# Optimization experiments

Measured on AMD Instinct MI355X. Metric: run time of the kernel, lower is better.

## Reference

```python
import jax, jax.numpy as jnp
import numpy as np

MODES = 20
WIDTH = 64
EPS = 1e-5


def spectral_conv(x, w1, w2, m1, m2):
    # x: [B, C, H, W] real; w1, w2: [Ci, Co, m1, m2, 2] (real/imag)
    B, C, H, W = x.shape
    xf = jnp.fft.rfft2(x, norm='ortho')  # [B, C, H, W//2+1] complex
    w1c = w1[..., 0] + 1j * w1[..., 1]
    w2c = w2[..., 0] + 1j * w2[..., 1]
    m1 = min(m1, H)
    m2 = min(m2, W // 2 + 1)
    top = jnp.einsum('bixy,ioxy->boxy', xf[:, :, :m1, :m2], w1c[:, :, :m1, :m2])
    bot = jnp.einsum('bixy,ioxy->boxy', xf[:, :, -m1:, :m2], w2c[:, :, :m1, :m2])
    out = jnp.zeros((B, w1.shape[1], H, W // 2 + 1), dtype=xf.dtype)
    out = out.at[:, :, :m1, :m2].set(top)
    out = out.at[:, :, H - m1:, :m2].set(bot)
    return jnp.fft.irfft2(out, s=(H, W), norm='ortho')


def batchnorm2d(x, gamma, beta):
    # training-mode BN over (B, H, W) per channel; x: [B, C, H, W]
    mean = jnp.mean(x, axis=(0, 2, 3), keepdims=True)
    var = jnp.var(x, axis=(0, 2, 3), keepdims=True)
    xn = (x - mean) * jax.lax.rsqrt(var + EPS)
    return xn * gamma[None, :, None, None] + beta[None, :, None, None]


def setup_inputs() -> dict:
    key = jax.random.key(0)
    ks = jax.random.split(key, 12)
    B, H, W, Tin2 = 8, 256, 256, 12
    scale = 1.0 / (WIDTH * WIDTH)
    return {
        'x': jax.random.normal(ks[0], (B, H, W, Tin2), jnp.float32),
        'fc0_w': jax.random.normal(ks[1], (Tin2, WIDTH), jnp.float32) * 0.1,
        'fc0_b': jnp.zeros((WIDTH,), jnp.float32),
        'sw1': scale * jax.random.normal(ks[2], (4, WIDTH, WIDTH, MODES, MODES, 2), jnp.float32),
        'sw2': scale * jax.random.normal(ks[3], (4, WIDTH, WIDTH, MODES, MODES, 2), jnp.float32),
        'cw': jax.random.normal(ks[4], (4, WIDTH, WIDTH), jnp.float32) * 0.1,
        'cb': jnp.zeros((4, WIDTH), jnp.float32),
        'bng': jnp.ones((4, WIDTH), jnp.float32),
        'bnb': jnp.zeros((4, WIDTH), jnp.float32),
        'fc1_w': jax.random.normal(ks[5], (WIDTH, 128), jnp.float32) * 0.1,
        'fc1_b': jnp.zeros((128,), jnp.float32),
        'fc2_w': jax.random.normal(ks[6], (128, 1), jnp.float32) * 0.1,
        'fc2_b': jnp.zeros((1,), jnp.float32),
    }


def reference(x, fc0_w, fc0_b, sw1, sw2, cw, cb, bng, bnb, fc1_w, fc1_b, fc2_w, fc2_b):
    # lift: [B, H, W, Tin+2] -> [B, C, H, W]
    h = jnp.einsum('bhwt,tc->bhwc', x, fc0_w) + fc0_b
    h = jnp.transpose(h, (0, 3, 1, 2))
    for l in range(4):
        spec = spectral_conv(h, sw1[l], sw2[l], MODES, MODES)
        lin = jnp.einsum('bihw,oi->bohw', h, cw[l]) + cb[l][None, :, None, None]
        h = batchnorm2d(spec + lin, bng[l], bnb[l])
        if l < 3:
            h = jax.nn.relu(h)
    h = jnp.transpose(h, (0, 2, 3, 1))  # [B, H, W, C]
    h = jax.nn.relu(jnp.einsum('bhwc,cd->bhwd', h, fc1_w) + fc1_b)
    out = jnp.einsum('bhwd,de->bhwe', h, fc2_w) + fc2_b
    return out
```

## Files before the change

### kernel.cpp

```cpp
#include <hip/hip_runtime.h>
#include <hip/hip_bf16.h>


__device__ __forceinline__ void gll16(const float* gsrc, float* ldst) {
    __builtin_amdgcn_global_load_lds(
        (const __attribute__((address_space(1))) void*)gsrc,
        (__attribute__((address_space(3))) void*)ldst, 16, 0, 0);
}

__device__ __forceinline__ unsigned bfp(float x) {
    unsigned u = __float_as_uint(x);
    return (u + 0x7fffu + ((u >> 16) & 1u)) >> 16;
}

__global__ __launch_bounds__(256) void init_k(const float* __restrict__ cw,
                                              float* __restrict__ costab, float* __restrict__ sintab,
                                              float* __restrict__ EAt, float* __restrict__ Tw,
                                              float* __restrict__ cwT, float* __restrict__ stats) {
    int idx = blockIdx.x * 256 + threadIdx.x;
    const float PH = 6.28318530717958647692f / 256.f;
    if (idx < 256) {
        float s, c; sincosf(idx * PH, &s, &c);
        costab[idx] = c; sintab[idx] = s;
    } else if (idx < 256 + 10240) {
        int e = idx - 256;
        int n = e >> 8, w = e & 255, ky = n >> 1;
        int r = (ky * w) & 255;
        float s, c; sincosf(r * PH, &s, &c);
        EAt[e] = (n & 1) ? -s : c;
    } else if (idx < 256 + 20480) {
        int e = idx - 10496;
        int kp = e >> 8, w = e & 255;
        int ky = kp >> 1, p = kp & 1;
        int r = (ky * w) & 255;
        float s, c; sincosf(r * PH, &s, &c);
        float v;
        if (ky == 0) v = p ? 0.f : (1.f / 16.f);
        else         v = p ? (-2.f / 16.f) * s : (2.f / 16.f) * c;
        Tw[e] = v;
    } else if (idx < 256 + 20480 + 16384) {
        int e = idx - 20736;
        int l = e >> 12, r2 = e & 4095;
        int i = r2 >> 6, o = r2 & 63;
        cwT[e] = cw[(l << 12) + (o << 6) + i];
    } else if (idx < 256 + 20480 + 16384 + 2048) {
        stats[idx - 37120] = 0.f;
    }
}

__global__ __launch_bounds__(256) void wtrans_k(const float* __restrict__ sw1,
                                                const float* __restrict__ sw2,
                                                unsigned int* __restrict__ wt) {
    int gid = blockIdx.x * 4 + (threadIdx.x >> 6);
    int o = threadIdx.x & 63;
    int xyc = gid % 25;
    int i = (gid / 25) & 63;
    int t2 = gid / 1600;
    const float* src = ((t2 & 1) ? sw2 : sw1) + (t2 >> 1) * 3276800;
    const float* sp = src + ((i * 64 + o) * 400 + xyc * 16) * 2;
    unsigned int* dp = wt + (size_t)(t2 * 400 + xyc * 16) * 4096 + i * 64 + o;
#pragma unroll
    for (int j = 0; j < 16; ++j) {
        float re = sp[2 * j], im = sp[2 * j + 1];
        dp[(size_t)j * 4096] = bfp(re) | (bfp(im) << 16);
    }
}

__global__ __launch_bounds__(256) void fc0_k(const float* __restrict__ x,
                                             const float* __restrict__ w,
                                             const float* __restrict__ bias,
                                             float* __restrict__ outb) {
    __shared__ float ws[768];
    __shared__ float bs[64];
    int tid = threadIdx.x;
    for (int i = tid; i < 768; i += 256) ws[i] = w[i];
    if (tid < 64) bs[tid] = bias[tid];
    __syncthreads();
    int pix = blockIdx.x * 256 + tid;
    int b = pix >> 16, hw = pix & 65535;
    float xv[12];
#pragma unroll
    for (int t = 0; t < 12; ++t) xv[t] = x[pix * 12 + t];
    int base = (b << 22) + hw;
    for (int c = 0; c < 64; ++c) {
        float a = bs[c];
#pragma unroll
        for (int t = 0; t < 12; ++t) a += xv[t] * ws[t * 64 + c];
        outb[base + (c << 16)] = a;
    }
}

__global__ __launch_bounds__(128) void dftw_k(float* __restrict__ X,
                                              const float* __restrict__ EAt,
                                              float* __restrict__ T,
                                              const float* __restrict__ statsl,
                                              const float* __restrict__ g,
                                              const float* __restrict__ bt,
                                              int fuse) {
    __shared__ __align__(16) float Xs[32 * 68];
    __shared__ __align__(16) float Est[40 * 32];
    int tid = threadIdx.x;
    int tm = tid >> 3, tn = tid & 7;
    int row0 = blockIdx.x << 6;
    float sc = 1.f, sh = 0.f;
    if (fuse) {
        int c = (row0 >> 8) & 63;
        float ssum = statsl[c] + statsl[128 + c] + statsl[256 + c] + statsl[384 + c];
        float ssq  = statsl[64 + c] + statsl[192 + c] + statsl[320 + c] + statsl[448 + c];
        float mean = ssum * (1.f / 524288.f);
        float var = ssq * (1.f / 524288.f) - mean * mean;
        sc = g[c] * rsqrtf(var + 1e-5f);
        sh = bt[c] - mean * sc;
    }
    float acc[4][5];
#pragma unroll
    for (int i = 0; i < 4; ++i)
#pragma unroll
        for (int j = 0; j < 5; ++j) acc[i][j] = 0.f;

#pragma unroll 1
    for (int kc = 0; kc < 256; kc += 32) {
        __syncthreads();
#pragma unroll
        for (int r = 0; r < 4; ++r) {
            int m = tm + (r << 4);
            float4 v = *(const float4*)&X[(row0 + m) * 256 + kc + (tn << 2)];
            if (fuse) {
                v.x = fmaxf(fmaf(v.x, sc, sh), 0.f);
                v.y = fmaxf(fmaf(v.y, sc, sh), 0.f);
                v.z = fmaxf(fmaf(v.z, sc, sh), 0.f);
                v.w = fmaxf(fmaf(v.w, sc, sh), 0.f);
                *(float4*)&X[(row0 + m) * 256 + kc + (tn << 2)] = v;
            }
            int kb = tn << 2;
            Xs[(kb + 0) * 68 + m] = v.x;
            Xs[(kb + 1) * 68 + m] = v.y;
            Xs[(kb + 2) * 68 + m] = v.z;
            Xs[(kb + 3) * 68 + m] = v.w;
        }
        for (int i = tid; i < 1280; i += 128) Est[i] = EAt[((i >> 5) << 8) + kc + (i & 31)];
        __syncthreads();
#pragma unroll 1
        for (int k4 = 0; k4 < 8; ++k4) {
            float4 e0 = *(const float4*)&Est[(tn * 5 + 0) * 32 + (k4 << 2)];
            float4 e1 = *(const float4*)&Est[(tn * 5 + 1) * 32 + (k4 << 2)];
            float4 e2 = *(const float4*)&Est[(tn * 5 + 2) * 32 + (k4 << 2)];
            float4 e3 = *(const float4*)&Est[(tn * 5 + 3) * 32 + (k4 << 2)];
            float4 e4 = *(const float4*)&Est[(tn * 5 + 4) * 32 + (k4 << 2)];
#pragma unroll
            for (int c2 = 0; c2 < 4; ++c2) {
                float4 a = *(const float4*)&Xs[((k4 << 2) + c2) * 68 + (tm << 2)];
                float ev0 = ((const float*)&e0)[c2];
                float ev1 = ((const float*)&e1)[c2];
                float ev2 = ((const float*)&e2)[c2];
                float ev3 = ((const float*)&e3)[c2];
                float ev4 = ((const float*)&e4)[c2];
                acc[0][0] += a.x * ev0; acc[1][0] += a.y * ev0; acc[2][0] += a.z * ev0; acc[3][0] += a.w * ev0;
                acc[0][1] += a.x * ev1; acc[1][1] += a.y * ev1; acc[2][1] += a.z * ev1; acc[3][1] += a.w * ev1;
                acc[0][2] += a.x * ev2; acc[1][2] += a.y * ev2; acc[2][2] += a.z * ev2; acc[3][2] += a.w * ev2;
                acc[0][3] += a.x * ev3; acc[1][3] += a.y * ev3; acc[2][3] += a.z * ev3; acc[3][3] += a.w * ev3;
                acc[0][4] += a.x * ev4; acc[1][4] += a.y * ev4; acc[2][4] += a.z * ev4; acc[3][4] += a.w * ev4;
            }
        }
    }
#pragma unroll
    for (int i = 0; i < 4; ++i) {
        int row = row0 + (tm << 2) + i;
#pragma unroll
        for (int j = 0; j < 5; ++j) T[row * 40 + tn * 5 + j] = acc[i][j];
    }
}

__global__ __launch_bounds__(1024) void dfth_k(const float* __restrict__ T,
                                               const float* __restrict__ ct, const float* __restrict__ st,
                                               float* __restrict__ XF) {
    __shared__ __align__(16) float Ts[10240];
    __shared__ float cts[256], sts[256];
    __shared__ float part[3][1600];
    int tid = threadIdx.x;
    int bc = blockIdx.x;
    for (int i = tid; i < 10240; i += 1024) Ts[i] = T[bc * 10240 + i];
    if (tid < 256) { cts[tid] = ct[tid]; sts[tid] = st[tid]; }
    __syncthreads();
    int gq = tid >> 8, t2 = tid & 255;
    float ar0 = 0, ai0 = 0, ar1 = 0, ai1 = 0, ar2 = 0, ai2 = 0, ar3 = 0, ai3 = 0;
    int kxi = t2 / 5, kyg = t2 % 5;
    if (t2 < 200) {
        int kxa = kxi < 20 ? kxi : kxi + 216;
        int h0 = gq << 6;
        int r = (kxa * h0) & 255;
#pragma unroll 1
        for (int hh = 0; hh < 64; ++hh) {
            int h = h0 + hh;
            float cc = cts[r], sv = sts[r];
            r = (r + kxa) & 255;
            float4 v0 = *(const float4*)&Ts[h * 40 + (kyg << 3)];
            float4 v1 = *(const float4*)&Ts[h * 40 + (kyg << 3) + 4];
            ar0 += v0.x * cc + v0.y * sv;  ai0 += v0.y * cc - v0.x * sv;
            ar1 += v0.z * cc + v0.w * sv;  ai1 += v0.w * cc - v0.z * sv;
            ar2 += v1.x * cc + v1.y * sv;  ai2 += v1.y * cc - v1.x * sv;
            ar3 += v1.z * cc + v1.w * sv;  ai3 += v1.w * cc - v1.z * sv;
        }
        if (gq) {
            float* p = &part[gq - 1][t2 * 8];
            p[0] = ar0; p[1] = ai0; p[2] = ar1; p[3] = ai1;
            p[4] = ar2; p[5] = ai2; p[6] = ar3; p[7] = ai3;
        }
    }
    __syncthreads();
    if (gq == 0 && t2 < 200) {
#pragma unroll
        for (int j = 0; j < 3; ++j) {
            const float* p = &part[j][t2 * 8];
            ar0 += p[0]; ai0 += p[1]; ar1 += p[2]; ai1 += p[3];
            ar2 += p[4]; ai2 += p[5]; ar3 += p[6]; ai3 += p[7];
        }
        int b = bc >> 6, c = bc & 63;
        const float s = 1.f / 256.f;
        int A = (b * 40 + kxi) * 20 + (kyg << 2);
        float2* O = (float2*)XF;
        O[(A + 0) * 64 + c] = make_float2(ar0 * s, ai0 * s);
        O[(A + 1) * 64 + c] = make_float2(ar1 * s, ai1 * s);
        O[(A + 2) * 64 + c] = make_float2(ar2 * s, ai2 * s);
        O[(A + 3) * 64 + c] = make_float2(ar3 * s, ai3 * s);
    }
}

__global__ __launch_bounds__(512) void eins_t_k(const float* __restrict__ XF,
                                                const unsigned int* __restrict__ wtl,
                                                float* __restrict__ YF) {
    __shared__ float xfs[1024];
    int tid = threadIdx.x;
    int x = blockIdx.x / 20, y = blockIdx.x % 20;
    for (int i = tid; i < 1024; i += 512) {
        int b = i >> 7, rr = i & 127;
        xfs[i] = XF[(b * 40 + x) * 2560 + y * 128 + rr];
    }
    __syncthreads();
    int b = tid >> 6, o = tid & 63;
    const unsigned int* wp = wtl + (size_t)(((x < 20 ? 0 : 400) + (x % 20) * 20 + y)) * 4096 + o;
    float ar = 0.f, ai = 0.f;
#pragma unroll 8
    for (int i = 0; i < 64; ++i) {
        unsigned int wv = wp[i << 6];
        float wr = __uint_as_float(wv << 16);
        float wi = __uint_as_float(wv & 0xffff0000u);
        float xr = xfs[(b << 7) + (i << 1)];
        float xi = xfs[(b << 7) + (i << 1) + 1];
        ar += xr * wr - xi * wi;
        ai += xr * wi + xi * wr;
    }
    ((float2*)YF)[((b * 40 + x) * 20 + y) * 64 + o] = make_float2(ar, ai);
}

__global__ __launch_bounds__(512) void eins_k(const float* __restrict__ XF,
                                              const float* __restrict__ w1, const float* __restrict__ w2,
                                              float* __restrict__ YF) {
    __shared__ float xfs[1024];
    int tid = threadIdx.x;
    int x = blockIdx.x / 20, y = blockIdx.x % 20;
    for (int i = tid; i < 1024; i += 512) {
        int b = i >> 7, rr = i & 127;
        xfs[i] = XF[(b * 40 + x) * 2560 + y * 128 + rr];
    }
    __syncthreads();
    int b = tid >> 6, o = tid & 63;
    const float* wp = (x < 20) ? (w1 + (x * 20 + y) * 2) : (w2 + ((x - 20) * 20 + y) * 2);
    float ar = 0.f, ai = 0.f;
#pragma unroll 8
    for (int i = 0; i < 64; ++i) {
        float2 wv = *(const float2*)&wp[(i * 64 + o) * 800];
        float xr = xfs[(b << 7) + (i << 1)];
        float xi = xfs[(b << 7) + (i << 1) + 1];
        ar += xr * wv.x - xi * wv.y;
        ai += xr * wv.y + xi * wv.x;
    }
    ((float2*)YF)[((b * 40 + x) * 20 + y) * 64 + o] = make_float2(ar, ai);
}

__global__ __launch_bounds__(256) void idfth_k(const float* __restrict__ YF,
                                               const float* __restrict__ ct, const float* __restrict__ st,
                                               float* __restrict__ Z) {
    __shared__ __align__(16) float yfs[1600];
    __shared__ float cts[256], sts[256];
    int tid = threadIdx.x;
    int bc = blockIdx.x;
    int b = bc >> 6, co = bc & 63;
    for (int i = tid; i < 800; i += 256) {
        int kx = i / 20, ky = i % 20;
        float2 v = ((const float2*)YF)[((b * 40 + kx) * 20 + ky) * 64 + co];
        yfs[kx * 40 + 2 * ky] = v.x;
        yfs[kx * 40 + 2 * ky + 1] = v.y;
    }
    cts[tid] = ct[tid]; sts[tid] = st[tid];
    __syncthreads();
    int h = tid;
    float accr[20], acci[20];
#pragma unroll
    for (int q = 0; q < 20; ++q) { accr[q] = 0.f; acci[q] = 0.f; }
#pragma unroll 1
    for (int kxi = 0; kxi < 40; ++kxi) {
        int kxa = kxi < 20 ? kxi : kxi + 216;
        int r = (kxa * h) & 255;
        float cc = cts[r], sv = sts[r];
#pragma unroll
        for (int q = 0; q < 10; ++q) {
            float4 v = *(const float4*)&yfs[kxi * 40 + (q << 2)];
            accr[2 * q]     += v.x * cc - v.y * sv;  acci[2 * q]     += v.x * sv + v.y * cc;
            accr[2 * q + 1] += v.z * cc - v.w * sv;  acci[2 * q + 1] += v.z * sv + v.w * cc;
        }
    }
    const float s = 1.f / 16.f;
    int base = (bc * 256 + h) * 40;
#pragma unroll
    for (int q = 0; q < 10; ++q) {
        float4 o4;
        o4.x = accr[2 * q] * s;     o4.y = acci[2 * q] * s;
        o4.z = accr[2 * q + 1] * s; o4.w = acci[2 * q + 1] * s;
        *(float4*)&Z[base + (q << 2)] = o4;
    }
}

#define FMA2(I, AV, J, B4) \
    acc[I][J].x += (AV) * B4.x; acc[I][J].y += (AV) * B4.y; \
    acc[I][J].z += (AV) * B4.z; acc[I][J].w += (AV) * B4.w;

#define FMA_COL(J, B4) \
    FMA2(0, a0.x, J, B4) FMA2(1, a0.y, J, B4) FMA2(2, a0.z, J, B4) FMA2(3, a0.w, J, B4) \
    FMA2(4, a1.x, J, B4) FMA2(5, a1.y, J, B4) FMA2(6, a1.z, J, B4) FMA2(7, a1.w, J, B4)

#define FMA_COLU(J, B4) \
    FMA2(0, au0.x, J, B4) FMA2(1, au0.y, J, B4) FMA2(2, au0.z, J, B4) FMA2(3, au0.w, J, B4) \
    FMA2(4, au1.x, J, B4) FMA2(5, au1.y, J, B4) FMA2(6, au1.z, J, B4) FMA2(7, au1.w, J, B4)

#define FMA_COLD(J, B4) \
    FMA2(0, ad0.x, J, B4) FMA2(1, ad0.y, J, B4) FMA2(2, ad0.z, J, B4) FMA2(3, ad0.w, J, B4) \
    FMA2(4, ad1.x, J, B4) FMA2(5, ad1.y, J, B4) FMA2(6, ad1.z, J, B4) FMA2(7, ad1.w, J, B4)

__global__ __launch_bounds__(256) void speclin_k(const float* __restrict__ hin,
                                                 const float* __restrict__ Z,
                                                 const float* __restrict__ cwTl,
                                                 const float* __restrict__ Tw,
                                                 const float* __restrict__ cbl,
                                                 float* __restrict__ pre,
                                                 float* __restrict__ statsl) {
    __shared__ __align__(16) float As[64 * 68];
    __shared__ __align__(16) float Zs[80 * 64];
    __shared__ __align__(16) float Bs[2][4096];
    int tid = threadIdx.x;
    int bid = blockIdx.x;
    int b = bid >> 7, hp = bid & 127;
    int h0 = hp << 1;
    int to = tid >> 5, tw = tid & 31;
    int o0 = to << 3;

#pragma unroll
    for (int t = 0; t < 4; ++t) {
        int i4 = tid + (t << 8);
        float4 v = *(const float4*)&cwTl[i4 << 2];
        float* d = &As[(i4 >> 4) * 68 + ((i4 & 15) << 2)];
        d[0] = v.x; d[1] = v.y; d[2] = v.z; d[3] = v.w;
    }
#pragma unroll
    for (int t = 0; t < 5; ++t) {
        int i4 = tid + (t << 8);
        int q = i4 % 10;
        int u = i4 / 10;
        int o = u & 63, r = u >> 6;
        float4 v = *(const float4*)&Z[(((b << 6) + o) * 256 + h0 + r) * 40 + (q << 2)];
        int base = ((r * 40 + (q << 2)) << 6) + o;
        Zs[base]       = v.x;
        Zs[base + 64]  = v.y;
        Zs[base + 128] = v.z;
        Zs[base + 192] = v.w;
    }
    const float* hrow = hin + (size_t)((((b << 6) << 8) + h0) << 8);
#pragma unroll
    for (int t = 0; t < 4; ++t) {
        int i4 = tid + (t << 8);
        int k = i4 >> 7, n4 = i4 & 127, r = n4 >> 6, w4 = n4 & 63;
        gll16(&hrow[(k << 16) + (r << 8) + (w4 << 2)], &Bs[0][i4 << 2]);
    }
    __syncthreads();

    float4 acc[8][4];
#pragma unroll
    for (int i = 0; i < 8; ++i)
#pragma unroll
        for (int j = 0; j < 4; ++j) acc[i][j] = make_float4(0.f, 0.f, 0.f, 0.f);

    int cur = 0;
#pragma unroll 1
    for (int ch = 0; ch < 8; ++ch) {
        if (ch < 7) {
#pragma unroll
            for (int t = 0; t < 4; ++t) {
                int i4 = tid + (t << 8);
                int k = i4 >> 7, n4 = i4 & 127, r = n4 >> 6, w4 = n4 & 63;
                gll16(&hrow[((((ch + 1) << 3) + k) << 16) + (r << 8) + (w4 << 2)],
                      &Bs[cur ^ 1][i4 << 2]);
            }
        } else {
#pragma unroll
            for (int t = 0; t < 2; ++t) {
                int i4 = tid + (t << 8);
                gll16(&Tw[i4 << 2], &Bs[cur ^ 1][i4 << 2]);
            }
        }
        const float* Bc = Bs[cur];
        const float* Ac = &As[(ch << 3) * 68 + o0];
#pragma unroll 1
        for (int kk = 0; kk < 8; ++kk) {
            float4 a0 = *(const float4*)&Ac[kk * 68];
            float4 a1 = *(const float4*)&Ac[kk * 68 + 4];
            float4 b0 = *(const float4*)&Bc[(kk << 9) + (tw << 2)];
            float4 b1 = *(const float4*)&Bc[(kk << 9) + 128 + (tw << 2)];
            FMA_COL(0, b0)
            FMA_COL(1, b1)
            float4 b2 = *(const float4*)&Bc[(kk << 9) + 256 + (tw << 2)];
            float4 b3 = *(const float4*)&Bc[(kk << 9) + 384 + (tw << 2)];
            FMA_COL(2, b2)
            FMA_COL(3, b3)
        }
        __syncthreads();
        cur ^= 1;
    }

#pragma unroll 1
    for (int ch = 0; ch < 5; ++ch) {
        if (ch < 4) {
#pragma unroll
            for (int t = 0; t < 2; ++t) {
                int i4 = tid + (t << 8);
                gll16(&Tw[(((ch + 1) << 3) << 8) + (i4 << 2)], &Bs[cur ^ 1][i4 << 2]);
            }
        }
        const float* Bc = Bs[cur];
#pragma unroll 1
        for (int kk = 0; kk < 8; ++kk) {
            int kp = (ch << 3) + kk;
            float4 b0 = *(const float4*)&Bc[(kk << 8) + (tw << 2)];
            float4 b1 = *(const float4*)&Bc[(kk << 8) + 128 + (tw << 2)];
            float4 au0 = *(const float4*)&Zs[(kp << 6) + o0];
            float4 au1 = *(const float4*)&Zs[(kp << 6) + o0 + 4];
            FMA_COLU(0, b0)
            FMA_COLU(1, b1)
            float4 ad0 = *(const float4*)&Zs[((40 + kp) << 6) + o0];
            float4 ad1 = *(const float4*)&Zs[((40 + kp) << 6) + o0 + 4];
            FMA_COLD(2, b0)
            FMA_COLD(3, b1)
        }
        __syncthreads();
        cur ^= 1;
    }

    float* srep = statsl + ((bid & 3) << 7);
#pragma unroll
    for (int i = 0; i < 8; ++i) {
        float cbv = cbl[o0 + i];
        float sum = 0.f, sq = 0.f;
#pragma unroll
        for (int j = 0; j < 4; ++j) {
            float4 v = acc[i][j];
            v.x += cbv; v.y += cbv; v.z += cbv; v.w += cbv;
            int row = h0 + (j >> 1);
            int wc = ((j & 1) << 7) + (tw << 2);
            *(float4*)&pre[(size_t)((((b << 6) + o0 + i) << 8) + row) * 256 + wc] = v;
            sum += v.x + v.y + v.z + v.w;
            sq  += v.x * v.x + v.y * v.y + v.z * v.z + v.w * v.w;
        }
        sum += __shfl_xor(sum, 1);  sq += __shfl_xor(sq, 1);
        sum += __shfl_xor(sum, 2);  sq += __shfl_xor(sq, 2);
        sum += __shfl_xor(sum, 4);  sq += __shfl_xor(sq, 4);
        sum += __shfl_xor(sum, 8);  sq += __shfl_xor(sq, 8);
        sum += __shfl_xor(sum, 16); sq += __shfl_xor(sq, 16);
        if ((tid & 31) == 0) {
            atomicAdd(&srep[o0 + i], sum);
            atomicAdd(&srep[64 + o0 + i], sq);
        }
    }
}

__global__ __launch_bounds__(256, 2) void fc12_k(const float* __restrict__ hin,
                                                 const float* __restrict__ statsl,
                                                 const float* __restrict__ g,
                                                 const float* __restrict__ bt,
                                                 const float* __restrict__ w1, const float* __restrict__ b1,
                                                 const float* __restrict__ w2, const float* __restrict__ b2,
                                                 float* __restrict__ out) {
    __shared__ __align__(16) float As[64 * 128];
    __shared__ __align__(16) float Bs[2][2048];
    __shared__ float scs[64], shs[64], bias2[128];
    __shared__ __align__(16) float red[4 * 256];
    int tid = threadIdx.x;
    int bh = blockIdx.x;
    int b = bh >> 8, h = bh & 255;
    int to = tid >> 4, tw = tid & 15;
    int d0 = to << 3;

    if (tid < 64) {
        float ssum = statsl[tid] + statsl[128 + tid] + statsl[256 + tid] + statsl[384 + tid];
        float ssq  = statsl[64 + tid] + statsl[192 + tid] + statsl[320 + tid] + statsl[448 + tid];
        float mean = ssum * (1.f / 524288.f);
        float var = ssq * (1.f / 524288.f) - mean * mean;
        float s = g[tid] * rsqrtf(var + 1e-5f);
        scs[tid] = s; shs[tid] = bt[tid] - mean * s;
    }
    __syncthreads();
    for (int i = tid; i < 8192; i += 256) As[i] = w1[i] * scs[i >> 7];
    if (tid < 128) {
        float a = b1[tid];
        for (int c = 0; c < 64; ++c) a += shs[c] * w1[c * 128 + tid];
        bias2[tid] = a;
    }
    const float* hrow = hin + ((size_t)(((b << 6) << 8) + h) << 8);
#pragma unroll
    for (int t = 0; t < 2; ++t) {
        int i4 = tid + (t << 8);
        gll16(&hrow[((i4 >> 6) << 16) + ((i4 & 63) << 2)], &Bs[0][i4 << 2]);
    }
    __syncthreads();

    float4 acc[8][4];
#pragma unroll
    for (int i = 0; i < 8; ++i)
#pragma unroll
        for (int j = 0; j < 4; ++j) acc[i][j] = make_float4(0.f, 0.f, 0.f, 0.f);

    int cur = 0;
#pragma unroll 1
    for (int ch = 0; ch < 8; ++ch) {
        if (ch < 7) {
#pragma unroll
            for (int t = 0; t < 2; ++t) {
                int i4 = tid + (t << 8);
                int k = i4 >> 6, w4 = (i4 & 63) << 2;
                gll16(&hrow[((((ch + 1) << 3) + k) << 16) + w4], &Bs[cur ^ 1][i4 << 2]);
            }
        }
        const float* Bc = Bs[cur];
#pragma unroll 2
        for (int kk = 0; kk < 8; ++kk) {
            int gk = (ch << 3) + kk;
            float4 a0 = *(const float4*)&As[(gk << 7) + d0];
            float4 a1 = *(const float4*)&As[(gk << 7) + d0 + 4];
            float4 b0 = *(const float4*)&Bc[(kk << 8) + (tw << 2)];
            float4 b1 = *(const float4*)&Bc[(kk << 8) + 64 + (tw << 2)];
            FMA_COL(0, b0)
            FMA_COL(1, b1)
            float4 b2 = *(const float4*)&Bc[(kk << 8) + 128 + (tw << 2)];
            float4 b3 = *(const float4*)&Bc[(kk << 8) + 192 + (tw << 2)];
            FMA_COL(2, b2)
            FMA_COL(3, b3)
        }
        __syncthreads();
        cur ^= 1;
    }

    float bb[8], wv[8];
#pragma unroll
    for (int i = 0; i < 8; ++i) { bb[i] = bias2[d0 + i]; wv[i] = w2[d0 + i]; }
    float4 p[4];
#pragma unroll
    for (int j = 0; j < 4; ++j) {
        float4 v = make_float4(0.f, 0.f, 0.f, 0.f);
#pragma unroll
        for (int i = 0; i < 8; ++i) {
            v.x += fmaxf(acc[i][j].x + bb[i], 0.f) * wv[i];
            v.y += fmaxf(acc[i][j].y + bb[i], 0.f) * wv[i];
            v.z += fmaxf(acc[i][j].z + bb[i], 0.f) * wv[i];
            v.w += fmaxf(acc[i][j].w + bb[i], 0.f) * wv[i];
        }
        v.x += __shfl_xor(v.x, 16); v.y += __shfl_xor(v.y, 16);
        v.z += __shfl_xor(v.z, 16); v.w += __shfl_xor(v.w, 16);
        v.x += __shfl_xor(v.x, 32); v.y += __shfl_xor(v.y, 32);
        v.z += __shfl_xor(v.z, 32); v.w += __shfl_xor(v.w, 32);
        p[j] = v;
    }
    int wave = tid >> 6;
    if ((tid & 63) < 16) {
#pragma unroll
        for (int j = 0; j < 4; ++j)
            *(float4*)&red[(wave << 8) + (j << 6) + (tw << 2)] = p[j];
    }
    __syncthreads();
    float s2 = b2[0] + red[tid] + red[256 + tid] + red[512 + tid] + red[768 + tid];
    out[(b * 256 + h) * 256 + tid] = s2;
}

extern "C" void kernel_launch(void* const* d_in, const int* in_sizes, int n_in,
                              void* d_out, int out_size, void* d_ws, size_t ws_size,
                              hipStream_t stream) {
    (void)in_sizes; (void)n_in; (void)out_size;
    const float* x     = (const float*)d_in[0];
    const float* fc0_w = (const float*)d_in[1];
    const float* fc0_b = (const float*)d_in[2];
    const float* sw1   = (const float*)d_in[3];
    const float* sw2   = (const float*)d_in[4];
    const float* cw    = (const float*)d_in[5];
    const float* cb    = (const float*)d_in[6];
    const float* bng   = (const float*)d_in[7];
    const float* bnb   = (const float*)d_in[8];
    const float* fc1_w = (const float*)d_in[9];
    const float* fc1_b = (const float*)d_in[10];
    const float* fc2_w = (const float*)d_in[11];
    const float* fc2_b = (const float*)d_in[12];
    float* out = (float*)d_out;

    float* ws = (float*)d_ws;
    float* hbuf   = ws;
    float* tz     = hbuf + 33554432;
    float* xf     = tz + 5242880;
    float* yf     = xf + 819200;
    float* costab = yf + 819200;
    float* sintab = costab + 256;
    float* EAt    = sintab + 256;
    float* Tw     = EAt + 10240;
    float* cwT    = Tw + 10240;
    float* stats  = cwT + 16384;
    unsigned* wt  = (unsigned*)(stats + 2048);

    size_t base_floats = 40473600 + 2048;
    int use_wt = (ws_size >= (base_floats + 13107200ull) * 4ull) ? 1 : 0;

    init_k<<<153, 256, 0, stream>>>(cw, costab, sintab, EAt, Tw, cwT, stats);
    if (use_wt) wtrans_k<<<3200, 256, 0, stream>>>(sw1, sw2, wt);
    fc0_k<<<2048, 256, 0, stream>>>(x, fc0_w, fc0_b, hbuf);

    for (int l = 0; l < 4; ++l) {
        if (l == 0)
            dftw_k<<<2048, 128, 0, stream>>>(hbuf, EAt, tz, stats, bng, bnb, 0);
        else
            dftw_k<<<2048, 128, 0, stream>>>(hbuf, EAt, tz, stats + (l - 1) * 512,
                                             bng + (l - 1) * 64, bnb + (l - 1) * 64, 1);
        dfth_k<<<512, 1024, 0, stream>>>(tz, costab, sintab, xf);
        if (use_wt)
            eins_t_k<<<800, 512, 0, stream>>>(xf, wt + (size_t)l * 2 * 400 * 4096, yf);
        else
            eins_k<<<800, 512, 0, stream>>>(xf, sw1 + l * 3276800, sw2 + l * 3276800, yf);
        idfth_k<<<512, 256, 0, stream>>>(yf, costab, sintab, tz);
        speclin_k<<<1024, 256, 0, stream>>>(hbuf, tz, cwT + l * 4096, Tw, cb + l * 64,
                                            hbuf, stats + l * 512);
    }
    fc12_k<<<2048, 256, 0, stream>>>(hbuf, stats + 3 * 512, bng + 3 * 64, bnb + 3 * 64,
                                     fc1_w, fc1_b, fc2_w, fc2_b, out);
}
```

Baseline: 1.200 ms.

## Enlarge row tiles in DFT-width and fc12 kernels for more reuse

The width-DFT kernel now computes 128 rows per block with an 8x5 register tile per thread. It gathers its input in registers and writes the transposed tile to shared memory with vectorized float4 stores, and the grid is halved. The fc12 head kernel now processes two image rows per 512-thread block, sharing the scaled fc1 weight load and bias setup across both rows. The reduction buffer now reuses the B staging memory. This amortizes per-block setup and the E/weight loads, at the cost of more registers per thread and fewer blocks in flight.

```diff
diff --git a/kernel.cpp b/kernel.cpp
--- a/kernel.cpp
+++ b/kernel.cpp
@@ -97,14 +97,15 @@
                                               const float* __restrict__ g,
                                               const float* __restrict__ bt,
                                               int fuse) {
-    __shared__ __align__(16) float Xs[32 * 68];
+    __shared__ __align__(16) float Xs[32 * 132];
     __shared__ __align__(16) float Est[40 * 32];
     int tid = threadIdx.x;
     int tm = tid >> 3, tn = tid & 7;
-    int row0 = blockIdx.x << 6;
+    int m0 = tm << 3;
+    int rowbase = blockIdx.x << 7;
     float sc = 1.f, sh = 0.f;
     if (fuse) {
-        int c = (row0 >> 8) & 63;
+        int c = (rowbase >> 8) & 63;
         float ssum = statsl[c] + statsl[128 + c] + statsl[256 + c] + statsl[384 + c];
         float ssq  = statsl[64 + c] + statsl[192 + c] + statsl[320 + c] + statsl[448 + c];
         float mean = ssum * (1.f / 524288.f);
@@ -112,31 +113,39 @@
         sc = g[c] * rsqrtf(var + 1e-5f);
         sh = bt[c] - mean * sc;
     }
-    float acc[4][5];
-#pragma unroll
-    for (int i = 0; i < 4; ++i)
+    float acc[8][5];
+#pragma unroll
+    for (int i = 0; i < 8; ++i)
 #pragma unroll
         for (int j = 0; j < 5; ++j) acc[i][j] = 0.f;
 
 #pragma unroll 1
     for (int kc = 0; kc < 256; kc += 32) {
-        __syncthreads();
-#pragma unroll
-        for (int r = 0; r < 4; ++r) {
-            int m = tm + (r << 4);
-            float4 v = *(const float4*)&X[(row0 + m) * 256 + kc + (tn << 2)];
+        float4 xv[8];
+#pragma unroll
+        for (int r = 0; r < 8; ++r) {
+            int row = rowbase + m0 + r;
+            float4 v = *(const float4*)&X[row * 256 + kc + (tn << 2)];
             if (fuse) {
                 v.x = fmaxf(fmaf(v.x, sc, sh), 0.f);
                 v.y = fmaxf(fmaf(v.y, sc, sh), 0.f);
                 v.z = fmaxf(fmaf(v.z, sc, sh), 0.f);
                 v.w = fmaxf(fmaf(v.w, sc, sh), 0.f);
-                *(float4*)&X[(row0 + m) * 256 + kc + (tn << 2)] = v;
+                *(float4*)&X[row * 256 + kc + (tn << 2)] = v;
             }
-            int kb = tn << 2;
-            Xs[(kb + 0) * 68 + m] = v.x;
-            Xs[(kb + 1) * 68 + m] = v.y;
-            Xs[(kb + 2) * 68 + m] = v.z;
-            Xs[(kb + 3) * 68 + m] = v.w;
+            xv[r] = v;
+        }
+        __syncthreads();
+#pragma unroll
+        for (int e = 0; e < 4; ++e) {
+            int k = (tn << 2) + e;
+            float4 w0, w1;
+            w0.x = ((const float*)&xv[0])[e]; w0.y = ((const float*)&xv[1])[e];
+            w0.z = ((const float*)&xv[2])[e]; w0.w = ((const float*)&xv[3])[e];
+            w1.x = ((const float*)&xv[4])[e]; w1.y = ((const float*)&xv[5])[e];
+            w1.z = ((const float*)&xv[6])[e]; w1.w = ((const float*)&xv[7])[e];
+            *(float4*)&Xs[k * 132 + m0] = w0;
+            *(float4*)&Xs[k * 132 + m0 + 4] = w1;
         }
         for (int i = tid; i < 1280; i += 128) Est[i] = EAt[((i >> 5) << 8) + kc + (i & 31)];
         __syncthreads();
@@ -149,25 +158,32 @@
             float4 e4 = *(const float4*)&Est[(tn * 5 + 4) * 32 + (k4 << 2)];
 #pragma unroll
             for (int c2 = 0; c2 < 4; ++c2) {
-                float4 a = *(const float4*)&Xs[((k4 << 2) + c2) * 68 + (tm << 2)];
+                int k = (k4 << 2) + c2;
+                float4 xa = *(const float4*)&Xs[k * 132 + m0];
+                float4 xb = *(const float4*)&Xs[k * 132 + m0 + 4];
                 float ev0 = ((const float*)&e0)[c2];
                 float ev1 = ((const float*)&e1)[c2];
                 float ev2 = ((const float*)&e2)[c2];
                 float ev3 = ((const float*)&e3)[c2];
                 float ev4 = ((const float*)&e4)[c2];
-                acc[0][0] += a.x * ev0; acc[1][0] += a.y * ev0; acc[2][0] += a.z * ev0; acc[3][0] += a.w * ev0;
-                acc[0][1] += a.x * ev1; acc[1][1] += a.y * ev1; acc[2][1] += a.z * ev1; acc[3][1] += a.w * ev1;
-                acc[0][2] += a.x * ev2; acc[1][2] += a.y * ev2; acc[2][2] += a.z * ev2; acc[3][2] += a.w * ev2;
-                acc[0][3] += a.x * ev3; acc[1][3] += a.y * ev3; acc[2][3] += a.z * ev3; acc[3][3] += a.w * ev3;
-                acc[0][4] += a.x * ev4; acc[1][4] += a.y * ev4; acc[2][4] += a.z * ev4; acc[3][4] += a.w * ev4;
+                acc[0][0] += xa.x * ev0; acc[1][0] += xa.y * ev0; acc[2][0] += xa.z * ev0; acc[3][0] += xa.w * ev0;
+                acc[4][0] += xb.x * ev0; acc[5][0] += xb.y * ev0; acc[6][0] += xb.z * ev0; acc[7][0] += xb.w * ev0;
+                acc[0][1] += xa.x * ev1; acc[1][1] += xa.y * ev1; acc[2][1] += xa.z * ev1; acc[3][1] += xa.w * ev1;
+                acc[4][1] += xb.x * ev1; acc[5][1] += xb.y * ev1; acc[6][1] += xb.z * ev1; acc[7][1] += xb.w * ev1;
+                acc[0][2] += xa.x * ev2; acc[1][2] += xa.y * ev2; acc[2][2] += xa.z * ev2; acc[3][2] += xa.w * ev2;
+                acc[4][2] += xb.x * ev2; acc[5][2] += xb.y * ev2; acc[6][2] += xb.z * ev2; acc[7][2] += xb.w * ev2;
+                acc[0][3] += xa.x * ev3; acc[1][3] += xa.y * ev3; acc[2][3] += xa.z * ev3; acc[3][3] += xa.w * ev3;
+                acc[4][3] += xb.x * ev3; acc[5][3] += xb.y * ev3; acc[6][3] += xb.z * ev3; acc[7][3] += xb.w * ev3;
+                acc[0][4] += xa.x * ev4; acc[1][4] += xa.y * ev4; acc[2][4] += xa.z * ev4; acc[3][4] += xa.w * ev4;
+                acc[4][4] += xb.x * ev4; acc[5][4] += xb.y * ev4; acc[6][4] += xb.z * ev4; acc[7][4] += xb.w * ev4;
             }
         }
     }
 #pragma unroll
-    for (int i = 0; i < 4; ++i) {
-        int row = row0 + (tm << 2) + i;
-#pragma unroll
-        for (int j = 0; j < 5; ++j) T[row * 40 + tn * 5 + j] = acc[i][j];
+    for (int r = 0; r < 8; ++r) {
+        int row = rowbase + m0 + r;
+#pragma unroll
+        for (int j = 0; j < 5; ++j) T[row * 40 + tn * 5 + j] = acc[r][j];
     }
 }
 
@@ -481,21 +497,21 @@
     }
 }
 
-__global__ __launch_bounds__(256, 2) void fc12_k(const float* __restrict__ hin,
-                                                 const float* __restrict__ statsl,
-                                                 const float* __restrict__ g,
-                                                 const float* __restrict__ bt,
-                                                 const float* __restrict__ w1, const float* __restrict__ b1,
-                                                 const float* __restrict__ w2, const float* __restrict__ b2,
-                                                 float* __restrict__ out) {
+__global__ __launch_bounds__(512) void fc12_k(const float* __restrict__ hin,
+                                              const float* __restrict__ statsl,
+                                              const float* __restrict__ g,
+                                              const float* __restrict__ bt,
+                                              const float* __restrict__ w1, const float* __restrict__ b1,
+                                              const float* __restrict__ w2, const float* __restrict__ b2,
+                                              float* __restrict__ out) {
     __shared__ __align__(16) float As[64 * 128];
-    __shared__ __align__(16) float Bs[2][2048];
+    __shared__ __align__(16) float Bs[2][4096];
     __shared__ float scs[64], shs[64], bias2[128];
-    __shared__ __align__(16) float red[4 * 256];
-    int tid = threadIdx.x;
-    int bh = blockIdx.x;
-    int b = bh >> 8, h = bh & 255;
-    int to = tid >> 4, tw = tid & 15;
+    int tid = threadIdx.x;
+    int bid = blockIdx.x;
+    int b = bid >> 7, hp = bid & 127;
+    int h0 = hp << 1;
+    int to = tid >> 5, tw = tid & 31;
     int d0 = to << 3;
 
     if (tid < 64) {
@@ -507,17 +523,18 @@
         scs[tid] = s; shs[tid] = bt[tid] - mean * s;
     }
     __syncthreads();
-    for (int i = tid; i < 8192; i += 256) As[i] = w1[i] * scs[i >> 7];
+    for (int i = tid; i < 8192; i += 512) As[i] = w1[i] * scs[i >> 7];
     if (tid < 128) {
         float a = b1[tid];
         for (int c = 0; c < 64; ++c) a += shs[c] * w1[c * 128 + tid];
         bias2[tid] = a;
     }
-    const float* hrow = hin + ((size_t)(((b << 6) << 8) + h) << 8);
+    const float* hrow = hin + (size_t)((((b << 6) << 8) + h0) << 8);
 #pragma unroll
     for (int t = 0; t < 2; ++t) {
-        int i4 = tid + (t << 8);
-        gll16(&hrow[((i4 >> 6) << 16) + ((i4 & 63) << 2)], &Bs[0][i4 << 2]);
+        int i4 = tid + (t << 9);
+        int k = i4 >> 7, n4 = i4 & 127, r = n4 >> 6, w4 = n4 & 63;
+        gll16(&hrow[(k << 16) + (r << 8) + (w4 << 2)], &Bs[0][i4 << 2]);
     }
     __syncthreads();
 
@@ -533,23 +550,24 @@
         if (ch < 7) {
 #pragma unroll
             for (int t = 0; t < 2; ++t) {
-                int i4 = tid + (t << 8);
-                int k = i4 >> 6, w4 = (i4 & 63) << 2;
-                gll16(&hrow[((((ch + 1) << 3) + k) << 16) + w4], &Bs[cur ^ 1][i4 << 2]);
+                int i4 = tid + (t << 9);
+                int k = i4 >> 7, n4 = i4 & 127, r = n4 >> 6, w4 = n4 & 63;
+                gll16(&hrow[((((ch + 1) << 3) + k) << 16) + (r << 8) + (w4 << 2)],
+                      &Bs[cur ^ 1][i4 << 2]);
             }
         }
         const float* Bc = Bs[cur];
-#pragma unroll 2
+#pragma unroll 1
         for (int kk = 0; kk < 8; ++kk) {
             int gk = (ch << 3) + kk;
             float4 a0 = *(const float4*)&As[(gk << 7) + d0];
             float4 a1 = *(const float4*)&As[(gk << 7) + d0 + 4];
-            float4 b0 = *(const float4*)&Bc[(kk << 8) + (tw << 2)];
-            float4 b1 = *(const float4*)&Bc[(kk << 8) + 64 + (tw << 2)];
+            float4 b0 = *(const float4*)&Bc[(kk << 9) + (tw << 2)];
+            float4 b1 = *(const float4*)&Bc[(kk << 9) + 128 + (tw << 2)];
             FMA_COL(0, b0)
             FMA_COL(1, b1)
-            float4 b2 = *(const float4*)&Bc[(kk << 8) + 128 + (tw << 2)];
-            float4 b3 = *(const float4*)&Bc[(kk << 8) + 192 + (tw << 2)];
+            float4 b2 = *(const float4*)&Bc[(kk << 9) + 256 + (tw << 2)];
+            float4 b3 = *(const float4*)&Bc[(kk << 9) + 384 + (tw << 2)];
             FMA_COL(2, b2)
             FMA_COL(3, b3)
         }
@@ -571,21 +589,26 @@
             v.z += fmaxf(acc[i][j].z + bb[i], 0.f) * wv[i];
             v.w += fmaxf(acc[i][j].w + bb[i], 0.f) * wv[i];
         }
-        v.x += __shfl_xor(v.x, 16); v.y += __shfl_xor(v.y, 16);
-        v.z += __shfl_xor(v.z, 16); v.w += __shfl_xor(v.w, 16);
         v.x += __shfl_xor(v.x, 32); v.y += __shfl_xor(v.y, 32);
         v.z += __shfl_xor(v.z, 32); v.w += __shfl_xor(v.w, 32);
         p[j] = v;
     }
+    float* red = &Bs[0][0];
     int wave = tid >> 6;
-    if ((tid & 63) < 16) {
+    if ((tid & 32) == 0) {
 #pragma unroll
         for (int j = 0; j < 4; ++j)
-            *(float4*)&red[(wave << 8) + (j << 6) + (tw << 2)] = p[j];
-    }
-    __syncthreads();
-    float s2 = b2[0] + red[tid] + red[256 + tid] + red[512 + tid] + red[768 + tid];
-    out[(b * 256 + h) * 256 + tid] = s2;
+            *(float4*)&red[(wave << 9) + (j << 7) + (tw << 2)] = p[j];
+    }
+    __syncthreads();
+    {
+        int n = tid;
+        float s2 = b2[0];
+#pragma unroll
+        for (int w8 = 0; w8 < 8; ++w8) s2 += red[(w8 << 9) + n];
+        int r = n >> 8, w = n & 255;
+        out[(b * 256 + h0 + r) * 256 + w] = s2;
+    }
 }
 
 extern "C" void kernel_launch(void* const* d_in, const int* in_sizes, int n_in,
@@ -629,9 +652,9 @@
 
     for (int l = 0; l < 4; ++l) {
         if (l == 0)
-            dftw_k<<<2048, 128, 0, stream>>>(hbuf, EAt, tz, stats, bng, bnb, 0);
+            dftw_k<<<1024, 128, 0, stream>>>(hbuf, EAt, tz, stats, bng, bnb, 0);
         else
-            dftw_k<<<2048, 128, 0, stream>>>(hbuf, EAt, tz, stats + (l - 1) * 512,
+            dftw_k<<<1024, 128, 0, stream>>>(hbuf, EAt, tz, stats + (l - 1) * 512,
                                              bng + (l - 1) * 64, bnb + (l - 1) * 64, 1);
         dfth_k<<<512, 1024, 0, stream>>>(tz, costab, sintab, xf);
         if (use_wt)
@@ -642,6 +665,6 @@
         speclin_k<<<1024, 256, 0, stream>>>(hbuf, tz, cwT + l * 4096, Tw, cb + l * 64,
                                             hbuf, stats + l * 512);
     }
-    fc12_k<<<2048, 256, 0, stream>>>(hbuf, stats + 3 * 512, bng + 3 * 64, bnb + 3 * 64,
+    fc12_k<<<1024, 512, 0, stream>>>(hbuf, stats + 3 * 512, bng + 3 * 64, bnb + 3 * 64,
                                      fc1_w, fc1_b, fc2_w, fc2_b, out);
 }
```

Result: slower. 1.259 ms (+4.9%).
